# Performance work log

Hardware: AMD Instinct MI355X
Metric: run time of the kernel (lower is better)

## Reference

```python
import jax, jax.numpy as jnp
import numpy as np

N, C, T, V = 16, 256, 400, 27
S, CI, O = 2, 64, 256      # num_subset, inter_channels, out_channels
OFFSET = 2                  # LearnedPositionalEmbedding offset
EPS = 1e-5                  # BatchNorm eps (inference/eval mode)


def _bn(x, g, b, m, v):
    # BatchNorm2d in eval mode: (x - mean)/sqrt(var+eps)*gamma + beta, per-channel
    return (x - m[None, :, None, None]) / jnp.sqrt(v[None, :, None, None] + EPS) \
        * g[None, :, None, None] + b[None, :, None, None]


def setup_inputs() -> dict:
    key = jax.random.key(0)
    ks = jax.random.split(key, 24)
    u = lambda k, s: jax.random.uniform(k, s, jnp.float32, 0.5, 1.5)
    r = lambda k, s, sc: jax.random.normal(k, s, jnp.float32) * sc
    d = {}
    d['x'] = jax.random.normal(ks[0], (N, C, T, V), jnp.float32)
    # learned positional embedding table: (num_frame + offset, num_node)
    d['pe'] = r(ks[1], (400 + OFFSET, V), 0.02)
    # in_nets: 1x1 conv C -> 2*S*CI
    d['in_w'] = r(ks[2], (2 * S * CI, C), 0.02)
    d['in_b'] = jnp.zeros((2 * S * CI,), jnp.float32)
    d['alphas'] = jnp.ones((1, S, 1, 1), jnp.float32)
    d['att0'] = jnp.ones((1, S, V, V), jnp.float32) / V   # attention0s
    # out_nets: 1x1 conv S*C -> O, then BN1
    d['out_w'] = r(ks[3], (O, S * C), 0.02)
    d['out_b'] = jnp.zeros((O,), jnp.float32)
    d['bn1_g'] = u(ks[4], (O,)); d['bn1_b'] = r(ks[5], (O,), 0.1)
    d['bn1_m'] = r(ks[6], (O,), 0.1); d['bn1_v'] = u(ks[7], (O,))
    # ff_nets: 1x1 conv O -> O, then BN2
    d['ff_w'] = r(ks[8], (O, O), 0.02)
    d['ff_b'] = jnp.zeros((O,), jnp.float32)
    d['bn2_g'] = u(ks[9], (O,)); d['bn2_b'] = r(ks[10], (O,), 0.1)
    d['bn2_m'] = r(ks[11], (O,), 0.1); d['bn2_v'] = u(ks[12], (O,))
    # out_nett: (3,1) temporal conv O -> O, then BN3
    d['t_w'] = r(ks[13], (O, O, 3, 1), 0.02)
    d['t_b'] = jnp.zeros((O,), jnp.float32)
    d['bn3_g'] = u(ks[14], (O,)); d['bn3_b'] = r(ks[15], (O,), 0.1)
    d['bn3_m'] = r(ks[16], (O,), 0.1); d['bn3_v'] = u(ks[17], (O,))
    return d


def reference(x, pe, in_w, in_b, alphas, att0, out_w, out_b,
              bn1_g, bn1_b, bn1_m, bn1_v, ff_w, ff_b,
              bn2_g, bn2_b, bn2_m, bn2_v, t_w, t_b,
              bn3_g, bn3_b, bn3_m, bn3_v):
    n, c, t, v = x.shape
    # learned positional embedding over frame index (shared across batch*channel)
    pos = pe[jnp.arange(t) + OFFSET]              # (T, V)
    y = x + pos[None, None, :, :]                 # (N, C, T, V)
    # in_nets 1x1 conv -> q, k
    qk = jnp.einsum('nctv,oc->notv', y, in_w) + in_b[None, :, None, None]
    qk = qk.reshape(n, 2 * S, CI, t, v)
    q, k = qk[:, :S], qk[:, S:]                   # (N, S, CI, T, V) each
    attn = jnp.einsum('nsctu,nsctv->nsuv', q, k) / (CI * t) * alphas + att0
    attn = jax.nn.softmax(attn, axis=-1)          # (N, S, V, V)  (dropout p=0)
    # re-aggregate values with original x
    y2 = jnp.einsum('nctu,nsuv->nsctv', x, attn).reshape(n, S * c, t, v)
    y2 = jnp.einsum('nctv,oc->notv', y2, out_w) + out_b[None, :, None, None]
    y2 = _bn(y2, bn1_g, bn1_b, bn1_m, bn1_v)
    y1 = jax.nn.leaky_relu(x + y2, 0.1)           # downs1 = identity (C==O)
    y2 = jnp.einsum('nctv,oc->notv', y1, ff_w) + ff_b[None, :, None, None]
    y2 = _bn(y2, bn2_g, bn2_b, bn2_m, bn2_v)
    y1 = jax.nn.leaky_relu(x + y2, 0.1)           # downs2 = identity
    # temporal branch (use_temporal_att=False): (3,1) conv + BN + residual
    z = jax.lax.conv_general_dilated(
        y1, t_w, window_strides=(1, 1), padding=((1, 1), (0, 0)),
        dimension_numbers=('NCHW', 'OIHW', 'NCHW')) + t_b[None, :, None, None]
    z = _bn(z, bn3_g, bn3_b, bn3_m, bn3_v)
    return jax.nn.leaky_relu(y1 + z, 0.1)         # downt2 = identity
```

## Files before the change

### kernel.cpp

```cpp
#include <hip/hip_runtime.h>
#include <hip/hip_bf16.h>
#include <cstddef>

#define NBATCH 16
#define CCH    256
#define TT     400
#define VV     27
#define TV     10800
#define EPSV   1e-5f
#define P2     10854

typedef __attribute__((ext_vector_type(8))) short  short8;
typedef __attribute__((ext_vector_type(4))) float  floatx4;

__device__ __forceinline__ unsigned short f2bu(float f) {
    __hip_bfloat16 h = __float2bfloat16(f);
    return *(unsigned short*)&h;
}
__device__ __forceinline__ float bu2f(unsigned short u) {
    union { float f; unsigned int i; } c; c.i = ((unsigned int)u) << 16; return c.f;
}
__device__ __forceinline__ void gl_lds16(const void* g, void* l) {
    __builtin_amdgcn_global_load_lds(
        (const __attribute__((address_space(1))) void*)g,
        (__attribute__((address_space(3))) void*)l, 16, 0, 0);
}

template<int KC, int MODE>
__global__ __launch_bounds__(256) void mfma_gemm(
    const unsigned short* __restrict__ X8,
    const unsigned short* __restrict__ W8,
    const float* __restrict__ bias,
    const float* __restrict__ bng, const float* __restrict__ bnb,
    const float* __restrict__ bnm, const float* __restrict__ bnv,
    const void* __restrict__ resv,
    float* __restrict__ outf,
    unsigned short* __restrict__ out8)
{
    constexpr int XPITCH = (MODE == 3) ? P2 : TV;
    constexpr int XOFF   = (MODE == 3) ? 27 : 0;
    constexpr int XROWS  = (MODE == 3) ? 32 : (KC / 8);
    constexpr int OPITCH = (MODE == 2) ? P2 : TV;
    constexpr int OOFF   = (MODE == 2) ? 27 : 0;

    __shared__ short Ws[4096];
    __shared__ short Xs[4096];
    __shared__ float scs[128], shs[128];

    const int tid  = threadIdx.x;
    const int wid  = tid >> 6;
    const int lane = tid & 63;
    const int quad = lane >> 4, col = lane & 15;
    const int n  = blockIdx.z;
    const int p0 = blockIdx.x * 128;
    const int o0 = blockIdx.y * 128;
    const int wo = (wid >> 1) * 64;
    const int wp = (wid & 1) * 64;

    const size_t nX = (size_t)n * XROWS * XPITCH;

    floatx4 acc[4][4];
    #pragma unroll
    for (int i = 0; i < 4; i++)
        #pragma unroll
        for (int j = 0; j < 4; j++)
            acc[i][j] = (floatx4){0.f, 0.f, 0.f, 0.f};

    for (int k0 = 0; k0 < KC; k0 += 32) {
        int c0 = k0, pshift = 0;
        if constexpr (MODE == 3) {
            int kt = k0 >> 8;
            c0 = k0 & 255;
            pshift = 27 * (kt - 1);
        }
        __syncthreads();
        #pragma unroll
        for (int q = 0; q < 2; q++) {
            const int ci = wid * 2 + q;
            const int kg = ci >> 1, half = ci & 1;
            const size_t woff = ((size_t)((k0 >> 3) + kg) * 256 + o0 + half * 64 + lane) * 8;
            gl_lds16(W8 + woff, Ws + ci * 512);
            const size_t xoff = (nX + (size_t)((c0 >> 3) + kg) * XPITCH
                                 + XOFF + p0 + pshift + half * 64 + lane) * 8;
            gl_lds16(X8 + xoff, Xs + ci * 512);
        }
        __syncthreads();
        short8 a[4], b[4];
        #pragma unroll
        for (int i = 0; i < 4; i++)
            a[i] = *(const short8*)&Ws[quad * 1024 + (wo + i * 16 + col) * 8];
        #pragma unroll
        for (int j = 0; j < 4; j++)
            b[j] = *(const short8*)&Xs[quad * 1024 + (wp + j * 16 + col) * 8];
        #pragma unroll
        for (int i = 0; i < 4; i++)
            #pragma unroll
            for (int j = 0; j < 4; j++)
                acc[i][j] = __builtin_amdgcn_mfma_f32_16x16x32_bf16(a[i], b[j], acc[i][j], 0, 0, 0);
    }

    __syncthreads();
    if (tid < 128) {
        const int o = o0 + tid;
        float sc, sh;
        if constexpr (MODE == 0) { sc = 1.f; sh = bias[o]; }
        else {
            const float g = bng[o], b2 = bnb[o], m = bnm[o], v2 = bnv[o];
            sc = g * rsqrtf(v2 + EPSV);
            sh = bias[o] * sc + b2 - m * sc;
        }
        scs[tid] = sc; shs[tid] = sh;
    }
    __syncthreads();

    const float* resf = (const float*)resv;
    const unsigned short* res8 = (const unsigned short*)resv;

    #pragma unroll
    for (int i = 0; i < 4; i++) {
        const int ol = wo + i * 16 + quad * 4;
        const int ob = o0 + ol;
        #pragma unroll
        for (int j = 0; j < 4; j++) {
            const int p = p0 + wp + j * 16 + col;
            if (p >= TV) continue;
            float v[4];
            #pragma unroll
            for (int r = 0; r < 4; r++)
                v[r] = acc[i][j][r] * scs[ol + r] + shs[ol + r];
            if constexpr (MODE == 3) {
                const size_t roff = ((size_t)n * 32 * P2 + (size_t)(ob >> 3) * P2 + 27 + p) * 8 + (ob & 7);
                union { unsigned long long u64; unsigned short us[4]; } rr;
                rr.u64 = *(const unsigned long long*)&res8[roff];
                #pragma unroll
                for (int r = 0; r < 4; r++) {
                    float t = v[r] + bu2f(rr.us[r]);
                    t = t > 0.f ? t : 0.1f * t;
                    outf[((size_t)n * 256 + ob + r) * TV + p] = t;
                }
            } else {
                union { unsigned long long u64; unsigned short us[4]; } pk;
                #pragma unroll
                for (int r = 0; r < 4; r++) {
                    float t = v[r];
                    if constexpr (MODE != 0) {
                        t += resf[((size_t)n * 256 + ob + r) * TV + p];
                        t = t > 0.f ? t : 0.1f * t;
                    }
                    pk.us[r] = f2bu(t);
                }
                *(unsigned long long*)&out8[((size_t)n * 32 * OPITCH
                    + (size_t)(ob >> 3) * OPITCH + OOFF + p) * 8 + (ob & 7)] = pk.u64;
            }
        }
    }
}

__global__ __launch_bounds__(256) void prep_xpe(
    const float* __restrict__ x, const float* __restrict__ pe,
    unsigned short* __restrict__ xpe8)
{
    const int p = blockIdx.x * 256 + threadIdx.x;
    const int cg = blockIdx.y, n = blockIdx.z;
    if (p >= TV) return;
    const float pev = pe[p + 54];
    const float* xp = x + ((size_t)n * 256 + cg * 8) * TV + p;
    union { unsigned short us[8]; uint4 q; } pk;
    #pragma unroll
    for (int r = 0; r < 8; r++)
        pk.us[r] = f2bu(xp[(size_t)r * TV] + pev);
    *(uint4*)&xpe8[(((size_t)n * 32 + cg) * TV + p) * 8] = pk.q;
}

__global__ void pack_w(const float* __restrict__ w, unsigned short* __restrict__ w8,
                       int KCc, int conv)
{
    const int idx = blockIdx.x * 256 + threadIdx.x;
    if (idx >= 256 * KCc) return;
    const int o = idx / KCc, k = idx - o * KCc;
    float v;
    if (conv) { const int c = k & 255, kt = k >> 8; v = w[((size_t)o * 256 + c) * 3 + kt]; }
    else v = w[(size_t)o * KCc + k];
    w8[((size_t)(k >> 3) * 256 + o) * 8 + (k & 7)] = f2bu(v);
}

__global__ void zero_pads(unsigned short* __restrict__ y1b8) {
    unsigned short* base = y1b8 + (size_t)blockIdx.x * P2 * 8;
    for (int i = threadIdx.x; i < 27 * 8; i += 256) {
        base[i] = 0;
        base[10827 * 8 + i] = 0;
    }
}

__global__ __launch_bounds__(256) void attn_logits_mfma(
    const unsigned short* __restrict__ qk8, float* __restrict__ logits)
{
    __shared__ float red[4][32][33];
    const int tid  = threadIdx.x;
    const int wid  = tid >> 6;
    const int lane = tid & 63;
    const int quad = lane >> 4, col = lane & 15;
    const int tch = blockIdx.x;
    const int ns  = blockIdx.y;
    const int n = ns >> 1, s = ns & 1;
    const int t0 = tch * 16 + wid * 4;

    const unsigned short* qb = qk8 + (size_t)(n * 32 + s * 8) * TV * 8;
    const unsigned short* kb = qk8 + (size_t)(n * 32 + 16 + s * 8) * TV * 8;

    floatx4 acc[2][2];
    #pragma unroll
    for (int i = 0; i < 2; i++)
        #pragma unroll
        for (int j = 0; j < 2; j++)
            acc[i][j] = (floatx4){0.f, 0.f, 0.f, 0.f};

    #pragma unroll
    for (int ti = 0; ti < 4; ti++) {
        const int t = t0 + ti;
        #pragma unroll
        for (int kk = 0; kk < 2; kk++) {
            const size_t ro = ((size_t)(kk * 4 + quad) * TV + t * 27 + col) * 8;
            const short8 a0 = *(const short8*)&qb[ro];
            const short8 a1 = *(const short8*)&qb[ro + 128];
            const short8 b0 = *(const short8*)&kb[ro];
            const short8 b1 = *(const short8*)&kb[ro + 128];
            acc[0][0] = __builtin_amdgcn_mfma_f32_16x16x32_bf16(a0, b0, acc[0][0], 0, 0, 0);
            acc[0][1] = __builtin_amdgcn_mfma_f32_16x16x32_bf16(a0, b1, acc[0][1], 0, 0, 0);
            acc[1][0] = __builtin_amdgcn_mfma_f32_16x16x32_bf16(a1, b0, acc[1][0], 0, 0, 0);
            acc[1][1] = __builtin_amdgcn_mfma_f32_16x16x32_bf16(a1, b1, acc[1][1], 0, 0, 0);
        }
    }

    #pragma unroll
    for (int i = 0; i < 2; i++)
        #pragma unroll
        for (int j = 0; j < 2; j++)
            #pragma unroll
            for (int r = 0; r < 4; r++)
                red[wid][i * 16 + quad * 4 + r][j * 16 + col] = acc[i][j][r];
    __syncthreads();
    for (int e = tid; e < 729; e += 256) {
        const int u = e / 27, v = e - u * 27;
        atomicAdd(&logits[(size_t)ns * 729 + e],
                  red[0][u][v] + red[1][u][v] + red[2][u][v] + red[3][u][v]);
    }
}

__global__ __launch_bounds__(64) void attn_softmax(
    const float* __restrict__ logits, const float* __restrict__ alphas,
    const float* __restrict__ att0, float* __restrict__ attn)
{
    const int ns = blockIdx.x;
    const int s = ns & 1;
    const int u = threadIdx.x;
    if (u < 27) {
        float row[27];
        const float alpha = alphas[s];
        const float inv_ct = 1.f / 25600.f;
        float m = -1e30f;
        for (int v = 0; v < 27; v++) {
            const float val = logits[(size_t)ns * 729 + u * 27 + v] * inv_ct * alpha
                            + att0[(size_t)(s * 27 + u) * 27 + v];
            row[v] = val;
            m = fmaxf(m, val);
        }
        float sum = 0.f;
        for (int v = 0; v < 27; v++) { row[v] = __expf(row[v] - m); sum += row[v]; }
        const float inv = 1.f / sum;
        for (int v = 0; v < 27; v++)
            attn[(size_t)ns * 729 + u * 27 + v] = row[v] * inv;
    }
}

__global__ __launch_bounds__(256) void xa_kernel(
    const float* __restrict__ x, const float* __restrict__ attn,
    unsigned short* __restrict__ xa8)
{
    __shared__ float at[2 * 729];
    __shared__ float xs[8][32 * 27];
    const int tid = threadIdx.x;
    const int tch = blockIdx.x, cg = blockIdx.y, n = blockIdx.z;
    const int t0 = tch * 32;
    const int nt = (t0 + 32 <= TT) ? 32 : (TT - t0);
    const int ne = nt * 27;

    for (int i = tid; i < 1458; i += 256) at[i] = attn[(size_t)n * 1458 + i];
    const float* xp = x + ((size_t)n * 256 + cg * 8) * TV + t0 * 27;
    for (int cc = 0; cc < 8; cc++)
        for (int i = tid; i < ne; i += 256) xs[cc][i] = xp[(size_t)cc * TV + i];
    __syncthreads();

    for (int s = 0; s < 2; s++) {
        unsigned short* op = xa8 + (((size_t)n * 64 + s * 32 + cg) * TV + t0 * 27) * 8;
        const float* a = &at[s * 729];
        for (int e = tid; e < ne; e += 256) {
            const int tl = e / 27, v = e - tl * 27;
            float acc[8] = {};
            for (int u = 0; u < 27; u++) {
                const float av = a[u * 27 + v];
                #pragma unroll
                for (int cc = 0; cc < 8; cc++) acc[cc] += xs[cc][tl * 27 + u] * av;
            }
            union { unsigned short us[8]; uint4 q; } pk;
            #pragma unroll
            for (int cc = 0; cc < 8; cc++) pk.us[cc] = f2bu(acc[cc]);
            *(uint4*)&op[(size_t)e * 8] = pk.q;
        }
    }
}

extern "C" void kernel_launch(void* const* d_in, const int* in_sizes, int n_in,
                              void* d_out, int out_size, void* d_ws, size_t ws_size,
                              hipStream_t stream) {
    const float* x      = (const float*)d_in[0];
    const float* pe     = (const float*)d_in[1];
    const float* in_w   = (const float*)d_in[2];
    const float* in_b   = (const float*)d_in[3];
    const float* alphas = (const float*)d_in[4];
    const float* att0   = (const float*)d_in[5];
    const float* out_w  = (const float*)d_in[6];
    const float* out_b  = (const float*)d_in[7];
    const float* bn1_g  = (const float*)d_in[8];
    const float* bn1_b  = (const float*)d_in[9];
    const float* bn1_m  = (const float*)d_in[10];
    const float* bn1_v  = (const float*)d_in[11];
    const float* ff_w   = (const float*)d_in[12];
    const float* ff_b   = (const float*)d_in[13];
    const float* bn2_g  = (const float*)d_in[14];
    const float* bn2_b  = (const float*)d_in[15];
    const float* bn2_m  = (const float*)d_in[16];
    const float* bn2_v  = (const float*)d_in[17];
    const float* t_w    = (const float*)d_in[18];
    const float* t_b    = (const float*)d_in[19];
    const float* bn3_g  = (const float*)d_in[20];
    const float* bn3_b  = (const float*)d_in[21];
    const float* bn3_m  = (const float*)d_in[22];
    const float* bn3_v  = (const float*)d_in[23];

    char* ws = (char*)d_ws;
    const size_t A_BYTES = (size_t)16 * 32 * TV * 8 * 2 + 8192;
    const size_t B_BYTES = (size_t)16 * 256 * TV * 4 + 8192;
    const size_t C_BYTES = (size_t)16 * 32 * P2 * 8 * 2 + 8192;
    unsigned short* xpe8 = (unsigned short*)ws;
    unsigned short* y1_8 = (unsigned short*)ws;
    unsigned short* qk8  = (unsigned short*)(ws + A_BYTES);
    unsigned short* xa8  = (unsigned short*)(ws + A_BYTES);
    unsigned short* y1b8 = (unsigned short*)(ws + A_BYTES + B_BYTES);
    char* D = ws + A_BYTES + B_BYTES + C_BYTES;
    float* logits = (float*)D;
    float* attn   = (float*)(D + 93440);
    unsigned short* w1_8 = (unsigned short*)(D + 2 * 93440);
    unsigned short* w4_8 = w1_8 + (size_t)256 * 256;
    unsigned short* w5_8 = w4_8 + (size_t)256 * 512;
    unsigned short* w6_8 = w5_8 + (size_t)256 * 256;

    pack_w<<<256, 256, 0, stream>>>(in_w,  w1_8, 256, 0);
    pack_w<<<512, 256, 0, stream>>>(out_w, w4_8, 512, 0);
    pack_w<<<256, 256, 0, stream>>>(ff_w,  w5_8, 256, 0);
    pack_w<<<768, 256, 0, stream>>>(t_w,   w6_8, 768, 1);
    prep_xpe<<<dim3(43, 32, 16), 256, 0, stream>>>(x, pe, xpe8);
    zero_pads<<<512, 256, 0, stream>>>(y1b8);

    dim3 gg((TV + 127) / 128, 2, NBATCH);

    mfma_gemm<256, 0><<<gg, 256, 0, stream>>>(
        xpe8, w1_8, in_b, nullptr, nullptr, nullptr, nullptr, nullptr, nullptr, qk8);

    hipMemsetAsync(logits, 0, (size_t)NBATCH * 2 * 729 * sizeof(float), stream);
    attn_logits_mfma<<<dim3(25, NBATCH * 2), 256, 0, stream>>>(qk8, logits);
    attn_softmax<<<NBATCH * 2, 64, 0, stream>>>(logits, alphas, att0, attn);

    xa_kernel<<<dim3(13, 32, 16), 256, 0, stream>>>(x, attn, xa8);

    mfma_gemm<512, 1><<<gg, 256, 0, stream>>>(
        xa8, w4_8, out_b, bn1_g, bn1_b, bn1_m, bn1_v, x, nullptr, y1_8);

    mfma_gemm<256, 2><<<gg, 256, 0, stream>>>(
        y1_8, w5_8, ff_b, bn2_g, bn2_b, bn2_m, bn2_v, x, nullptr, y1b8);

    mfma_gemm<768, 3><<<gg, 256, 0, stream>>>(
        y1b8, w6_8, t_b, bn3_g, bn3_b, bn3_m, bn3_v, y1b8, (float*)d_out, nullptr);
}
```

Measured before the change: 980.6 us.

## Compute x·attn aggregation with bf16 MFMA instead of scalar FMA loops

Replaces the scalar LDS-based xa kernel with an MFMA version. Each wave loads the attention matrix into bf16 B fragments and the x rows (converted to bf16) into A fragments, then issues 16x16x32 MFMAs over the node dimension padded to 32. The goal is to cut the scalar FMA cost and the LDS staging of this stage. In exchange, x and attn are rounded to bf16 before the product, and the x loads and the 8-byte output stores are strided and uncoalesced.

```diff
diff --git a/kernel.cpp b/kernel.cpp
--- a/kernel.cpp
+++ b/kernel.cpp
@@ -273,39 +273,59 @@
     }
 }
 
-__global__ __launch_bounds__(256) void xa_kernel(
+__global__ __launch_bounds__(256) void xa_mfma(
     const float* __restrict__ x, const float* __restrict__ attn,
     unsigned short* __restrict__ xa8)
 {
-    __shared__ float at[2 * 729];
-    __shared__ float xs[8][32 * 27];
-    const int tid = threadIdx.x;
-    const int tch = blockIdx.x, cg = blockIdx.y, n = blockIdx.z;
-    const int t0 = tch * 32;
-    const int nt = (t0 + 32 <= TT) ? 32 : (TT - t0);
-    const int ne = nt * 27;
-
-    for (int i = tid; i < 1458; i += 256) at[i] = attn[(size_t)n * 1458 + i];
-    const float* xp = x + ((size_t)n * 256 + cg * 8) * TV + t0 * 27;
-    for (int cc = 0; cc < 8; cc++)
-        for (int i = tid; i < ne; i += 256) xs[cc][i] = xp[(size_t)cc * TV + i];
-    __syncthreads();
-
+    const int tid  = threadIdx.x;
+    const int wid  = tid >> 6;
+    const int lane = tid & 63;
+    const int quad = lane >> 4, col = lane & 15;
+    const int tch = blockIdx.x;
+    const int c0  = blockIdx.y * 16;
+    const int n   = blockIdx.z;
+
+    short8 bf[2][2];
+    #pragma unroll
     for (int s = 0; s < 2; s++) {
-        unsigned short* op = xa8 + (((size_t)n * 64 + s * 32 + cg) * TV + t0 * 27) * 8;
-        const float* a = &at[s * 729];
-        for (int e = tid; e < ne; e += 256) {
-            const int tl = e / 27, v = e - tl * 27;
-            float acc[8] = {};
-            for (int u = 0; u < 27; u++) {
-                const float av = a[u * 27 + v];
-                #pragma unroll
-                for (int cc = 0; cc < 8; cc++) acc[cc] += xs[cc][tl * 27 + u] * av;
+        const float* ab = attn + (size_t)(n * 2 + s) * 729;
+        #pragma unroll
+        for (int vt = 0; vt < 2; vt++) {
+            const int v = vt * 16 + col;
+            #pragma unroll
+            for (int e = 0; e < 8; e++) {
+                const int u = quad * 8 + e;
+                bf[s][vt][e] = (u < 27 && v < 27) ? (short)f2bu(ab[u * 27 + v]) : (short)0;
             }
-            union { unsigned short us[8]; uint4 q; } pk;
+        }
+    }
+
+    const float* xrow = x + ((size_t)n * 256 + c0 + col) * TV;
+
+    #pragma unroll
+    for (int ti = 0; ti < 4; ti++) {
+        const int t = tch * 16 + wid * 4 + ti;
+        short8 af;
+        #pragma unroll
+        for (int e = 0; e < 8; e++) {
+            const int u = quad * 8 + e;
+            af[e] = (u < 27) ? (short)f2bu(xrow[t * 27 + u]) : (short)0;
+        }
+        #pragma unroll
+        for (int s = 0; s < 2; s++) {
             #pragma unroll
-            for (int cc = 0; cc < 8; cc++) pk.us[cc] = f2bu(acc[cc]);
-            *(uint4*)&op[(size_t)e * 8] = pk.q;
+            for (int vt = 0; vt < 2; vt++) {
+                floatx4 d = __builtin_amdgcn_mfma_f32_16x16x32_bf16(
+                    af, bf[s][vt], (floatx4){0.f, 0.f, 0.f, 0.f}, 0, 0, 0);
+                const int v = vt * 16 + col;
+                if (v < 27) {
+                    const size_t cgg = (size_t)n * 64 + s * 32 + (c0 >> 3) + (quad >> 1);
+                    union { unsigned long long u64; unsigned short us[4]; } pk;
+                    #pragma unroll
+                    for (int r = 0; r < 4; r++) pk.us[r] = f2bu(d[r]);
+                    *(unsigned long long*)&xa8[(cgg * TV + t * 27 + v) * 8 + (quad & 1) * 4] = pk.u64;
+                }
+            }
         }
     }
 }
@@ -371,7 +391,7 @@
     attn_logits_mfma<<<dim3(25, NBATCH * 2), 256, 0, stream>>>(qk8, logits);
     attn_softmax<<<NBATCH * 2, 64, 0, stream>>>(logits, alphas, att0, attn);
 
-    xa_kernel<<<dim3(13, 32, 16), 256, 0, stream>>>(x, attn, xa8);
+    xa_mfma<<<dim3(25, 16, 16), 256, 0, stream>>>(x, attn, xa8);
 
     mfma_gemm<512, 1><<<gg, 256, 0, stream>>>(
         xa8, w4_8, out_b, bn1_g, bn1_b, bn1_m, bn1_v, x, nullptr, y1_8);
```

Result: faster. 908.0 us (-7.4%).
